# Performance work log

Hardware: AMD Instinct MI355X
Metric: run time of the kernel (lower is better)

The kernel has to match this reference:

```python
import jax, jax.numpy as jnp
import numpy as np

B, S, D = 1, 4096, 512
QK_DIM, N_HEADS = 512, 8
HEAD_DIM = QK_DIM // N_HEADS


def setup_inputs() -> dict:
    key = jax.random.key(0)
    ks = jax.random.split(key, 9)
    s_in = 1.0 / np.sqrt(D)
    s_v = 1.0 / np.sqrt(QK_DIM)
    return {
        "x": jax.random.normal(ks[0], (B, S, D), dtype=jnp.float32),
        # torch nn.Linear convention: weight (out_features, in_features)
        "Wq": jax.random.uniform(ks[1], (QK_DIM, D), jnp.float32, -s_in, s_in),
        "bq": jax.random.uniform(ks[2], (QK_DIM,), jnp.float32, -s_in, s_in),
        "Wk": jax.random.uniform(ks[3], (QK_DIM, D), jnp.float32, -s_in, s_in),
        "bk": jax.random.uniform(ks[4], (QK_DIM,), jnp.float32, -s_in, s_in),
        "Wv": jax.random.uniform(ks[5], (QK_DIM, D), jnp.float32, -s_in, s_in),
        "bv": jax.random.uniform(ks[6], (QK_DIM,), jnp.float32, -s_in, s_in),
        "Wo": jax.random.uniform(ks[7], (D, QK_DIM), jnp.float32, -s_v, s_v),
        "bo": jax.random.uniform(ks[8], (D,), jnp.float32, -s_v, s_v),
    }


def reference(x, Wq, bq, Wk, bk, Wv, bv, Wo, bo):
    # Faithful to source: tokens flattened over batch*seq before head split.
    n = x.shape[0] * x.shape[1]  # B*S
    Q = (x @ Wq.T + bq).reshape(n, N_HEADS, HEAD_DIM).transpose(1, 0, 2)  # (H, N, hd)
    K = (x @ Wk.T + bk).reshape(n, N_HEADS, HEAD_DIM).transpose(1, 0, 2)
    V = (x @ Wv.T + bv).reshape(n, N_HEADS, HEAD_DIM).transpose(1, 0, 2)
    scores = jnp.einsum("hnd,hmd->hnm", Q, K) / np.sqrt(HEAD_DIM).astype(np.float32)
    attn = jax.nn.softmax(scores, axis=-1)                # (H, N, N) materialized
    ctx = jnp.einsum("hnm,hmd->hnd", attn, V)             # (H, N, hd)
    ctx = ctx.transpose(1, 0, 2).reshape(n, QK_DIM)       # (N, qk_dim)
    return ctx @ Wo.T + bo                                # (N, input_dim)
```

## Files before the change

### kernel.cpp

```cpp
#include <hip/hip_runtime.h>
#include <math.h>

#define N_TOK 4096
#define DMODEL 512
#define NH 8
#define HD 64

typedef __attribute__((ext_vector_type(4))) float f32x4;
typedef __attribute__((ext_vector_type(8))) _Float16 f16x8;
typedef __attribute__((ext_vector_type(4))) _Float16 f16x4;

#define MFMA16(A, B, C) __builtin_amdgcn_mfma_f32_16x16x32_f16(A, B, C, 0, 0, 0)

__global__ __launch_bounds__(256) void cast_x(const float* __restrict__ x,
                                              _Float16* __restrict__ X16) {
    int i = (blockIdx.x * 256 + threadIdx.x) * 8;
    f32x4 a = *(const f32x4*)&x[i];
    f32x4 b = *(const f32x4*)&x[i + 4];
    f16x8 o = {(_Float16)a[0], (_Float16)a[1], (_Float16)a[2], (_Float16)a[3],
               (_Float16)b[0], (_Float16)b[1], (_Float16)b[2], (_Float16)b[3]};
    *(f16x8*)&X16[i] = o;
}

__global__ __launch_bounds__(256) void qkv_gemm(const _Float16* __restrict__ X16,
                                                const float* __restrict__ Wq,
                                                const float* __restrict__ bq,
                                                const float* __restrict__ Wk,
                                                const float* __restrict__ bk,
                                                const float* __restrict__ Wv,
                                                const float* __restrict__ bv,
                                                _Float16* __restrict__ Q16,
                                                _Float16* __restrict__ K16,
                                                _Float16* __restrict__ VT16) {
    __shared__ __align__(16) _Float16 As[128][72];
    __shared__ __align__(16) _Float16 Ws[64][72];
    int z = blockIdx.z;
    const float* W = (z == 0) ? Wq : (z == 1) ? Wk : Wv;
    const float* bias = (z == 0) ? bq : (z == 1) ? bk : bv;

    int n0 = blockIdx.x * 128, o0 = blockIdx.y * 64;
    int t = threadIdx.x;
    int w = t >> 6, l = t & 63, quad = l >> 4, ln = l & 15;
    int sr = t >> 3, sc = (t & 7) * 8;
    int wr = t >> 2, wc = (t & 3) * 16;

    const _Float16* Abase = X16 + (size_t)n0 * DMODEL;
    const float* Wbase = W + (size_t)o0 * DMODEL;

    f32x4 acc[2][4] = {};

    f16x8 pa[4];
    f32x4 pw[4];
#pragma unroll
    for (int r = 0; r < 4; r++) pa[r] = *(const f16x8*)&Abase[(size_t)(sr + r * 32) * DMODEL + sc];
#pragma unroll
    for (int r = 0; r < 4; r++) pw[r] = *(const f32x4*)&Wbase[(size_t)wr * DMODEL + wc + r * 4];

    for (int k0 = 0; k0 < DMODEL; k0 += 64) {
        __syncthreads();
#pragma unroll
        for (int r = 0; r < 4; r++) *(f16x8*)&As[sr + r * 32][sc] = pa[r];
        {
            f16x8 w0 = {(_Float16)pw[0][0], (_Float16)pw[0][1], (_Float16)pw[0][2],
                        (_Float16)pw[0][3], (_Float16)pw[1][0], (_Float16)pw[1][1],
                        (_Float16)pw[1][2], (_Float16)pw[1][3]};
            f16x8 w1 = {(_Float16)pw[2][0], (_Float16)pw[2][1], (_Float16)pw[2][2],
                        (_Float16)pw[2][3], (_Float16)pw[3][0], (_Float16)pw[3][1],
                        (_Float16)pw[3][2], (_Float16)pw[3][3]};
            *(f16x8*)&Ws[wr][wc] = w0;
            *(f16x8*)&Ws[wr][wc + 8] = w1;
        }
        __syncthreads();

        int k1 = k0 + 64;
        if (k1 < DMODEL) {
#pragma unroll
            for (int r = 0; r < 4; r++)
                pa[r] = *(const f16x8*)&Abase[(size_t)(sr + r * 32) * DMODEL + k1 + sc];
#pragma unroll
            for (int r = 0; r < 4; r++)
                pw[r] = *(const f32x4*)&Wbase[(size_t)wr * DMODEL + k1 + wc + r * 4];
        }

#pragma unroll
        for (int ks = 0; ks < 2; ks++) {
            f16x8 af0 = *(const f16x8*)&As[w * 32 + ln][ks * 32 + quad * 8];
            f16x8 af1 = *(const f16x8*)&As[w * 32 + 16 + ln][ks * 32 + quad * 8];
#pragma unroll
            for (int c = 0; c < 4; c++) {
                f16x8 bf = *(const f16x8*)&Ws[c * 16 + ln][ks * 32 + quad * 8];
                acc[0][c] = MFMA16(af0, bf, acc[0][c]);
                acc[1][c] = MFMA16(af1, bf, acc[1][c]);
            }
        }
    }

    int h = o0 >> 6;
    const float QS = 0.125f * 1.44269504088896340736f;

    if (z < 2) {
        float sc_ = (z == 0) ? QS : 1.0f;
#pragma unroll
        for (int c = 0; c < 4; c++) {
            float bv_ = bias[o0 + c * 16 + ln];
#pragma unroll
            for (int rt = 0; rt < 2; rt++)
#pragma unroll
                for (int i = 0; i < 4; i++) {
                    int lr = w * 32 + rt * 16 + quad * 4 + i;
                    As[lr][c * 16 + ln] = (_Float16)((acc[rt][c][i] + bv_) * sc_);
                }
        }
        __syncthreads();
        _Float16* dst = (z == 0) ? Q16 : K16;
#pragma unroll
        for (int k = 0; k < 4; k++) {
            int row = k * 32 + (t >> 3), col = (t & 7) * 8;
            *(f16x8*)&dst[((size_t)h * N_TOK + n0 + row) * HD + col] =
                *(const f16x8*)&As[row][col];
        }
    } else {
        __syncthreads();
        _Float16(*Et)[136] = (_Float16(*)[136]) & As[0][0];
#pragma unroll
        for (int c = 0; c < 4; c++) {
            float bv_ = bias[o0 + c * 16 + ln];
#pragma unroll
            for (int rt = 0; rt < 2; rt++)
#pragma unroll
                for (int i = 0; i < 4; i++) {
                    int np = (w >> 1) * 64 + (quad * 4 + i) * 4 + (w & 1) * 2 + rt;
                    Et[c * 16 + ln][np] = (_Float16)(acc[rt][c][i] + bv_);
                }
        }
        __syncthreads();
#pragma unroll
        for (int k = 0; k < 4; k++) {
            int d = k * 16 + (t >> 4), col = (t & 15) * 8;
            *(f16x8*)&VT16[((size_t)h * HD + d) * N_TOK + n0 + col] =
                *(const f16x8*)&Et[d][col];
        }
    }
}

__global__ __launch_bounds__(1024) void flash_mfma(const _Float16* __restrict__ Q16,
                                                   const _Float16* __restrict__ K16,
                                                   const _Float16* __restrict__ VT16,
                                                   _Float16* __restrict__ OP,
                                                   float* __restrict__ LS) {
    __shared__ __align__(16) _Float16 Ks[2][64][72];
    __shared__ __align__(16) _Float16 Vs[2][64][72];
    __shared__ __align__(16) _Float16 Ps[16][32][72];

    int t = threadIdx.x;
    int w = t >> 6, l = t & 63, quad = l >> 4, ln = l & 15;
    int bid = blockIdx.x;
    int h = bid & 7;
    int qt = (bid >> 3) & 7;
    int s = bid >> 6;
    int q0 = qt * 512 + w * 32;
    int m_start = s * 1024;

    f16x8 qf[2][2];
#pragma unroll
    for (int rt = 0; rt < 2; rt++) {
        const _Float16* qp = &Q16[((size_t)h * N_TOK + q0 + rt * 16 + ln) * HD + quad * 8];
        qf[rt][0] = *(const f16x8*)qp;
        qf[rt][1] = *(const f16x8*)(qp + 32);
    }

    f32x4 oacc[2][4] = {};
    f32x4 lsum[2] = {};

    const _Float16* kbase = K16 + (size_t)h * N_TOK * HD;
    const _Float16* vbase = VT16 + (size_t)h * HD * N_TOK;
    int g = t >> 9, tt = t & 511;
    int srow = tt >> 3, scol = (tt & 7) * 8;

    f16x8 pkv;
    if (g == 0)
        pkv = *(const f16x8*)(kbase + (size_t)(m_start + srow) * HD + scol);
    else
        pkv = *(const f16x8*)(vbase + (size_t)srow * N_TOK + m_start + scol);

    for (int it = 0; it < 16; it++) {
        int m0 = m_start + it * 64;
        int p = it & 1;
        if (g == 0)
            *(f16x8*)&Ks[p][srow][scol] = pkv;
        else
            *(f16x8*)&Vs[p][srow][scol] = pkv;
        __syncthreads();

        if (it < 15) {
            int m1 = m0 + 64;
            if (g == 0)
                pkv = *(const f16x8*)(kbase + (size_t)(m1 + srow) * HD + scol);
            else
                pkv = *(const f16x8*)(vbase + (size_t)srow * N_TOK + m1 + scol);
        }

        f16x8 kb[4][2];
#pragma unroll
        for (int c = 0; c < 4; c++) {
            kb[c][0] = *(const f16x8*)&Ks[p][c * 16 + ln][quad * 8];
            kb[c][1] = *(const f16x8*)&Ks[p][c * 16 + ln][32 + quad * 8];
        }
#pragma unroll
        for (int rt = 0; rt < 2; rt++) {
            f32x4 sacc[4] = {};
#pragma unroll
            for (int c = 0; c < 4; c++) {
                sacc[c] = MFMA16(qf[rt][0], kb[c][0], sacc[c]);
                sacc[c] = MFMA16(qf[rt][1], kb[c][1], sacc[c]);
            }
#pragma unroll
            for (int i = 0; i < 4; i++) {
                float p0 = __builtin_exp2f(sacc[0][i]);
                float p1 = __builtin_exp2f(sacc[1][i]);
                float p2 = __builtin_exp2f(sacc[2][i]);
                float p3 = __builtin_exp2f(sacc[3][i]);
                lsum[rt][i] += (p0 + p1) + (p2 + p3);
                f16x4 pvv = {(_Float16)p0, (_Float16)p1, (_Float16)p2, (_Float16)p3};
                *(f16x4*)&Ps[w][rt * 16 + quad * 4 + i][ln * 4] = pvv;
            }
        }
        f16x8 vb[4][2];
#pragma unroll
        for (int c = 0; c < 4; c++) {
            vb[c][0] = *(const f16x8*)&Vs[p][c * 16 + ln][quad * 8];
            vb[c][1] = *(const f16x8*)&Vs[p][c * 16 + ln][32 + quad * 8];
        }
#pragma unroll
        for (int rt = 0; rt < 2; rt++) {
            f16x8 a0 = *(const f16x8*)&Ps[w][rt * 16 + ln][quad * 8];
            f16x8 a1 = *(const f16x8*)&Ps[w][rt * 16 + ln][32 + quad * 8];
#pragma unroll
            for (int c = 0; c < 4; c++) {
                oacc[rt][c] = MFMA16(a0, vb[c][0], oacc[rt][c]);
                oacc[rt][c] = MFMA16(a1, vb[c][1], oacc[rt][c]);
            }
        }
    }

#pragma unroll
    for (int d = 1; d < 16; d <<= 1)
#pragma unroll
        for (int rt = 0; rt < 2; rt++)
#pragma unroll
            for (int i = 0; i < 4; i++) lsum[rt][i] += __shfl_xor(lsum[rt][i], d, 64);

    _Float16* obase = OP + (size_t)s * N_TOK * DMODEL;
#pragma unroll
    for (int rt = 0; rt < 2; rt++)
#pragma unroll
        for (int c = 0; c < 4; c++)
#pragma unroll
            for (int i = 0; i < 4; i++) {
                int r = q0 + rt * 16 + quad * 4 + i;
                obase[(size_t)r * DMODEL + h * HD + c * 16 + ln] = (_Float16)oacc[rt][c][i];
            }
    if (ln == 0) {
#pragma unroll
        for (int rt = 0; rt < 2; rt++)
#pragma unroll
            for (int i = 0; i < 4; i++) {
                int r = q0 + rt * 16 + quad * 4 + i;
                LS[((size_t)s * NH + h) * N_TOK + r] = lsum[rt][i];
            }
    }
}

__global__ __launch_bounds__(256) void combine(const _Float16* __restrict__ OP,
                                               const float* __restrict__ LS,
                                               _Float16* __restrict__ CTX16) {
    const size_t PSTR = (size_t)N_TOK * DMODEL;
    int idx = blockIdx.x * 256 + threadIdx.x;
    int col8 = idx & 63;
    int n = idx >> 6;
    int h = col8 >> 3;
    const float* ls = LS + (size_t)h * N_TOK + n;
    float lt = (ls[0] + ls[NH * N_TOK]) + (ls[2 * NH * N_TOK] + ls[3 * NH * N_TOK]);
    float inv = 1.0f / lt;
    size_t base = (size_t)n * DMODEL + col8 * 8;
    f16x8 a0 = *(const f16x8*)&OP[base];
    f16x8 a1 = *(const f16x8*)&OP[PSTR + base];
    f16x8 a2 = *(const f16x8*)&OP[2 * PSTR + base];
    f16x8 a3 = *(const f16x8*)&OP[3 * PSTR + base];
    f16x8 o;
#pragma unroll
    for (int j = 0; j < 8; j++)
        o[j] = (_Float16)((((float)a0[j] + (float)a1[j]) + ((float)a2[j] + (float)a3[j])) * inv);
    *(f16x8*)&CTX16[base] = o;
}

__global__ __launch_bounds__(256) void out_gemm(const _Float16* __restrict__ A,
                                                const float* __restrict__ Wo,
                                                const float* __restrict__ bo,
                                                float* __restrict__ out) {
    __shared__ __align__(16) _Float16 As[64][72];
    __shared__ __align__(16) _Float16 Ws[64][72];
    int n0 = blockIdx.x * 64, o0 = blockIdx.y * 64;
    int t = threadIdx.x;
    int w = t >> 6, l = t & 63, quad = l >> 4, ln = l & 15;
    int sr = t >> 2, sc = (t & 3) * 16;

    const _Float16* Abase = A + (size_t)n0 * DMODEL;
    const float* Wbase = Wo + (size_t)o0 * DMODEL;

    f32x4 acc[4] = {};

    f16x8 pa0 = *(const f16x8*)&Abase[(size_t)sr * DMODEL + sc];
    f16x8 pa1 = *(const f16x8*)&Abase[(size_t)sr * DMODEL + sc + 8];
    f32x4 pw[4];
#pragma unroll
    for (int r = 0; r < 4; r++) pw[r] = *(const f32x4*)&Wbase[(size_t)sr * DMODEL + sc + r * 4];

    for (int k0 = 0; k0 < DMODEL; k0 += 64) {
        __syncthreads();
        *(f16x8*)&As[sr][sc] = pa0;
        *(f16x8*)&As[sr][sc + 8] = pa1;
        {
            f16x8 w0 = {(_Float16)pw[0][0], (_Float16)pw[0][1], (_Float16)pw[0][2],
                        (_Float16)pw[0][3], (_Float16)pw[1][0], (_Float16)pw[1][1],
                        (_Float16)pw[1][2], (_Float16)pw[1][3]};
            f16x8 w1 = {(_Float16)pw[2][0], (_Float16)pw[2][1], (_Float16)pw[2][2],
                        (_Float16)pw[2][3], (_Float16)pw[3][0], (_Float16)pw[3][1],
                        (_Float16)pw[3][2], (_Float16)pw[3][3]};
            *(f16x8*)&Ws[sr][sc] = w0;
            *(f16x8*)&Ws[sr][sc + 8] = w1;
        }
        __syncthreads();

        int k1 = k0 + 64;
        if (k1 < DMODEL) {
            pa0 = *(const f16x8*)&Abase[(size_t)sr * DMODEL + k1 + sc];
            pa1 = *(const f16x8*)&Abase[(size_t)sr * DMODEL + k1 + sc + 8];
#pragma unroll
            for (int r = 0; r < 4; r++)
                pw[r] = *(const f32x4*)&Wbase[(size_t)sr * DMODEL + k1 + sc + r * 4];
        }

#pragma unroll
        for (int ks = 0; ks < 2; ks++) {
            f16x8 af = *(const f16x8*)&As[w * 16 + ln][ks * 32 + quad * 8];
#pragma unroll
            for (int c = 0; c < 4; c++) {
                f16x8 bf = *(const f16x8*)&Ws[c * 16 + ln][ks * 32 + quad * 8];
                acc[c] = MFMA16(af, bf, acc[c]);
            }
        }
    }

#pragma unroll
    for (int c = 0; c < 4; c++) {
        float bv_ = bo[o0 + c * 16 + ln];
#pragma unroll
        for (int i = 0; i < 4; i++) {
            int r = n0 + w * 16 + quad * 4 + i;
            out[(size_t)r * DMODEL + o0 + c * 16 + ln] = acc[c][i] + bv_;
        }
    }
}

extern "C" void kernel_launch(void* const* d_in, const int* in_sizes, int n_in,
                              void* d_out, int out_size, void* d_ws, size_t ws_size,
                              hipStream_t stream) {
    const float* x  = (const float*)d_in[0];
    const float* Wq = (const float*)d_in[1];
    const float* bq = (const float*)d_in[2];
    const float* Wk = (const float*)d_in[3];
    const float* bk = (const float*)d_in[4];
    const float* Wv = (const float*)d_in[5];
    const float* bv = (const float*)d_in[6];
    const float* Wo = (const float*)d_in[7];
    const float* bo = (const float*)d_in[8];
    float* out = (float*)d_out;

    char* ws = (char*)d_ws;
    _Float16* X16  = (_Float16*)(ws);
    _Float16* Q16  = (_Float16*)(ws + (4u << 20));
    _Float16* K16  = (_Float16*)(ws + (8u << 20));
    _Float16* VT16 = (_Float16*)(ws + (12u << 20));
    _Float16* OP   = (_Float16*)(ws + (16u << 20));
    float*    LSp  = (float*)   (ws + (32u << 20));
    _Float16* CTX  = (_Float16*)(ws + (33u << 20));

    cast_x<<<1024, 256, 0, stream>>>(x, X16);

    qkv_gemm<<<dim3(32, 8, 3), 256, 0, stream>>>(X16, Wq, bq, Wk, bk, Wv, bv,
                                                 Q16, K16, VT16);

    flash_mfma<<<dim3(256), 1024, 0, stream>>>(Q16, K16, VT16, OP, LSp);

    combine<<<1024, 256, 0, stream>>>(OP, LSp, CTX);

    out_gemm<<<dim3(64, 8), 256, 0, stream>>>(CTX, Wo, bo, out);
}
```

Measured before the change: 155.2 us.

## Fuse split-KV combine into output GEMM and merge QKV projections per block

The separate combine kernel is removed. The output GEMM now loads the four split partial outputs and their row sums, normalizes them in registers and stages the result as its A tile, so the intermediate context buffer round trip and one launch go away. The QKV GEMM now computes Q, K and V in one 768-thread block that shares a single staged X tile across the three weight matrices, and both GEMMs switch to double-buffered shared memory with one barrier per k-step. In exchange, the output GEMM reads four times as much A data per k-step and both kernels use larger blocks and more shared memory, which can lower occupancy.

```diff
diff --git a/kernel.cpp b/kernel.cpp
--- a/kernel.cpp
+++ b/kernel.cpp
@@ -22,7 +22,7 @@
     *(f16x8*)&X16[i] = o;
 }
 
-__global__ __launch_bounds__(256) void qkv_gemm(const _Float16* __restrict__ X16,
+__global__ __launch_bounds__(768) void qkv_gemm(const _Float16* __restrict__ X16,
                                                 const float* __restrict__ Wq,
                                                 const float* __restrict__ bq,
                                                 const float* __restrict__ Wk,
@@ -32,113 +32,154 @@
                                                 _Float16* __restrict__ Q16,
                                                 _Float16* __restrict__ K16,
                                                 _Float16* __restrict__ VT16) {
-    __shared__ __align__(16) _Float16 As[128][72];
-    __shared__ __align__(16) _Float16 Ws[64][72];
-    int z = blockIdx.z;
-    const float* W = (z == 0) ? Wq : (z == 1) ? Wk : Wv;
-    const float* bias = (z == 0) ? bq : (z == 1) ? bk : bv;
-
-    int n0 = blockIdx.x * 128, o0 = blockIdx.y * 64;
+    __shared__ __align__(16) _Float16 smem[46080];
+    _Float16* AsB = smem;
+    _Float16* WsB = smem + 18432;
+
     int t = threadIdx.x;
     int w = t >> 6, l = t & 63, quad = l >> 4, ln = l & 15;
-    int sr = t >> 3, sc = (t & 7) * 8;
-    int wr = t >> 2, wc = (t & 3) * 16;
+    int z = w >> 2, ww = w & 3;
+    int n0 = blockIdx.x * 128, o0 = blockIdx.y * 64;
+    int h = o0 >> 6;
+
+    const float* biasz = (z == 0) ? bq : (z == 1) ? bk : bv;
+
+    f32x4 acc[2][4] = {};
+
+    bool isA = (t < 256);
+    int asr = t >> 3, asc = (t & 7) * 8;
+    int tt = t - 256;
+    int wr = tt >> 3, wc = (tt & 7) * 8;
 
     const _Float16* Abase = X16 + (size_t)n0 * DMODEL;
-    const float* Wbase = W + (size_t)o0 * DMODEL;
-
-    f32x4 acc[2][4] = {};
+    const float* W0 = Wq + (size_t)o0 * DMODEL;
+    const float* W1 = Wk + (size_t)o0 * DMODEL;
+    const float* W2 = Wv + (size_t)o0 * DMODEL;
 
     f16x8 pa[4];
-    f32x4 pw[4];
-#pragma unroll
-    for (int r = 0; r < 4; r++) pa[r] = *(const f16x8*)&Abase[(size_t)(sr + r * 32) * DMODEL + sc];
-#pragma unroll
-    for (int r = 0; r < 4; r++) pw[r] = *(const f32x4*)&Wbase[(size_t)wr * DMODEL + wc + r * 4];
-
-    for (int k0 = 0; k0 < DMODEL; k0 += 64) {
+    f32x4 pw[3][2];
+    if (isA) {
+#pragma unroll
+        for (int r = 0; r < 4; r++)
+            pa[r] = *(const f16x8*)&Abase[(size_t)(asr + r * 32) * DMODEL + asc];
+    } else {
+        pw[0][0] = *(const f32x4*)&W0[(size_t)wr * DMODEL + wc];
+        pw[0][1] = *(const f32x4*)&W0[(size_t)wr * DMODEL + wc + 4];
+        pw[1][0] = *(const f32x4*)&W1[(size_t)wr * DMODEL + wc];
+        pw[1][1] = *(const f32x4*)&W1[(size_t)wr * DMODEL + wc + 4];
+        pw[2][0] = *(const f32x4*)&W2[(size_t)wr * DMODEL + wc];
+        pw[2][1] = *(const f32x4*)&W2[(size_t)wr * DMODEL + wc + 4];
+    }
+
+    for (int it = 0; it < 8; it++) {
+        int p = it & 1;
+        if (isA) {
+#pragma unroll
+            for (int r = 0; r < 4; r++)
+                *(f16x8*)&AsB[(size_t)(p * 128 + asr + r * 32) * 72 + asc] = pa[r];
+        } else {
+#pragma unroll
+            for (int zt = 0; zt < 3; zt++) {
+                f16x8 wv_ = {(_Float16)pw[zt][0][0], (_Float16)pw[zt][0][1],
+                             (_Float16)pw[zt][0][2], (_Float16)pw[zt][0][3],
+                             (_Float16)pw[zt][1][0], (_Float16)pw[zt][1][1],
+                             (_Float16)pw[zt][1][2], (_Float16)pw[zt][1][3]};
+                *(f16x8*)&WsB[(size_t)((p * 3 + zt) * 64 + wr) * 72 + wc] = wv_;
+            }
+        }
         __syncthreads();
-#pragma unroll
-        for (int r = 0; r < 4; r++) *(f16x8*)&As[sr + r * 32][sc] = pa[r];
-        {
-            f16x8 w0 = {(_Float16)pw[0][0], (_Float16)pw[0][1], (_Float16)pw[0][2],
-                        (_Float16)pw[0][3], (_Float16)pw[1][0], (_Float16)pw[1][1],
-                        (_Float16)pw[1][2], (_Float16)pw[1][3]};
-            f16x8 w1 = {(_Float16)pw[2][0], (_Float16)pw[2][1], (_Float16)pw[2][2],
-                        (_Float16)pw[2][3], (_Float16)pw[3][0], (_Float16)pw[3][1],
-                        (_Float16)pw[3][2], (_Float16)pw[3][3]};
-            *(f16x8*)&Ws[wr][wc] = w0;
-            *(f16x8*)&Ws[wr][wc + 8] = w1;
-        }
-        __syncthreads();
-
-        int k1 = k0 + 64;
+
+        int k1 = (it + 1) * 64;
         if (k1 < DMODEL) {
-#pragma unroll
-            for (int r = 0; r < 4; r++)
-                pa[r] = *(const f16x8*)&Abase[(size_t)(sr + r * 32) * DMODEL + k1 + sc];
-#pragma unroll
-            for (int r = 0; r < 4; r++)
-                pw[r] = *(const f32x4*)&Wbase[(size_t)wr * DMODEL + k1 + wc + r * 4];
+            if (isA) {
+#pragma unroll
+                for (int r = 0; r < 4; r++)
+                    pa[r] = *(const f16x8*)&Abase[(size_t)(asr + r * 32) * DMODEL + k1 + asc];
+            } else {
+                pw[0][0] = *(const f32x4*)&W0[(size_t)wr * DMODEL + k1 + wc];
+                pw[0][1] = *(const f32x4*)&W0[(size_t)wr * DMODEL + k1 + wc + 4];
+                pw[1][0] = *(const f32x4*)&W1[(size_t)wr * DMODEL + k1 + wc];
+                pw[1][1] = *(const f32x4*)&W1[(size_t)wr * DMODEL + k1 + wc + 4];
+                pw[2][0] = *(const f32x4*)&W2[(size_t)wr * DMODEL + k1 + wc];
+                pw[2][1] = *(const f32x4*)&W2[(size_t)wr * DMODEL + k1 + wc + 4];
+            }
         }
 
 #pragma unroll
         for (int ks = 0; ks < 2; ks++) {
-            f16x8 af0 = *(const f16x8*)&As[w * 32 + ln][ks * 32 + quad * 8];
-            f16x8 af1 = *(const f16x8*)&As[w * 32 + 16 + ln][ks * 32 + quad * 8];
+            f16x8 af0 = *(const f16x8*)&AsB[(size_t)(p * 128 + ww * 32 + ln) * 72 +
+                                            ks * 32 + quad * 8];
+            f16x8 af1 = *(const f16x8*)&AsB[(size_t)(p * 128 + ww * 32 + 16 + ln) * 72 +
+                                            ks * 32 + quad * 8];
 #pragma unroll
             for (int c = 0; c < 4; c++) {
-                f16x8 bf = *(const f16x8*)&Ws[c * 16 + ln][ks * 32 + quad * 8];
+                f16x8 bf = *(const f16x8*)&WsB[(size_t)((p * 3 + z) * 64 + c * 16 + ln) * 72 +
+                                               ks * 32 + quad * 8];
                 acc[0][c] = MFMA16(af0, bf, acc[0][c]);
                 acc[1][c] = MFMA16(af1, bf, acc[1][c]);
             }
         }
     }
 
-    int h = o0 >> 6;
+    __syncthreads();
+
     const float QS = 0.125f * 1.44269504088896340736f;
+    _Float16* Qs = smem;
+    _Float16* Ksep = smem + 9216;
+    _Float16* Vt = smem + 18432;
 
     if (z < 2) {
+        _Float16* st = (z == 0) ? Qs : Ksep;
         float sc_ = (z == 0) ? QS : 1.0f;
 #pragma unroll
         for (int c = 0; c < 4; c++) {
-            float bv_ = bias[o0 + c * 16 + ln];
+            float bv_ = biasz[o0 + c * 16 + ln];
 #pragma unroll
             for (int rt = 0; rt < 2; rt++)
 #pragma unroll
                 for (int i = 0; i < 4; i++) {
-                    int lr = w * 32 + rt * 16 + quad * 4 + i;
-                    As[lr][c * 16 + ln] = (_Float16)((acc[rt][c][i] + bv_) * sc_);
+                    int lr = ww * 32 + rt * 16 + quad * 4 + i;
+                    st[(size_t)lr * 72 + c * 16 + ln] =
+                        (_Float16)((acc[rt][c][i] + bv_) * sc_);
                 }
         }
-        __syncthreads();
-        _Float16* dst = (z == 0) ? Q16 : K16;
+    } else {
+#pragma unroll
+        for (int c = 0; c < 4; c++) {
+            float bv_ = biasz[o0 + c * 16 + ln];
+#pragma unroll
+            for (int rt = 0; rt < 2; rt++)
+#pragma unroll
+                for (int i = 0; i < 4; i++) {
+                    int np = (ww >> 1) * 64 + (quad * 4 + i) * 4 + (ww & 1) * 2 + rt;
+                    Vt[(size_t)(c * 16 + ln) * 136 + np] = (_Float16)(acc[rt][c][i] + bv_);
+                }
+        }
+    }
+    __syncthreads();
+
+    if (t < 256) {
 #pragma unroll
         for (int k = 0; k < 4; k++) {
             int row = k * 32 + (t >> 3), col = (t & 7) * 8;
-            *(f16x8*)&dst[((size_t)h * N_TOK + n0 + row) * HD + col] =
-                *(const f16x8*)&As[row][col];
+            *(f16x8*)&Q16[((size_t)h * N_TOK + n0 + row) * HD + col] =
+                *(const f16x8*)&Qs[(size_t)row * 72 + col];
+        }
+    } else if (t < 512) {
+        int u = t - 256;
+#pragma unroll
+        for (int k = 0; k < 4; k++) {
+            int row = k * 32 + (u >> 3), col = (u & 7) * 8;
+            *(f16x8*)&K16[((size_t)h * N_TOK + n0 + row) * HD + col] =
+                *(const f16x8*)&Ksep[(size_t)row * 72 + col];
         }
     } else {
-        __syncthreads();
-        _Float16(*Et)[136] = (_Float16(*)[136]) & As[0][0];
-#pragma unroll
-        for (int c = 0; c < 4; c++) {
-            float bv_ = bias[o0 + c * 16 + ln];
-#pragma unroll
-            for (int rt = 0; rt < 2; rt++)
-#pragma unroll
-                for (int i = 0; i < 4; i++) {
-                    int np = (w >> 1) * 64 + (quad * 4 + i) * 4 + (w & 1) * 2 + rt;
-                    Et[c * 16 + ln][np] = (_Float16)(acc[rt][c][i] + bv_);
-                }
-        }
-        __syncthreads();
+        int u = t - 512;
 #pragma unroll
         for (int k = 0; k < 4; k++) {
-            int d = k * 16 + (t >> 4), col = (t & 15) * 8;
+            int d = k * 16 + (u >> 4), col = (u & 15) * 8;
             *(f16x8*)&VT16[((size_t)h * HD + d) * N_TOK + n0 + col] =
-                *(const f16x8*)&Et[d][col];
+                *(const f16x8*)&Vt[(size_t)d * 136 + col];
         }
     }
 }
@@ -271,82 +312,88 @@
     }
 }
 
-__global__ __launch_bounds__(256) void combine(const _Float16* __restrict__ OP,
-                                               const float* __restrict__ LS,
-                                               _Float16* __restrict__ CTX16) {
-    const size_t PSTR = (size_t)N_TOK * DMODEL;
-    int idx = blockIdx.x * 256 + threadIdx.x;
-    int col8 = idx & 63;
-    int n = idx >> 6;
-    int h = col8 >> 3;
-    const float* ls = LS + (size_t)h * N_TOK + n;
-    float lt = (ls[0] + ls[NH * N_TOK]) + (ls[2 * NH * N_TOK] + ls[3 * NH * N_TOK]);
-    float inv = 1.0f / lt;
-    size_t base = (size_t)n * DMODEL + col8 * 8;
-    f16x8 a0 = *(const f16x8*)&OP[base];
-    f16x8 a1 = *(const f16x8*)&OP[PSTR + base];
-    f16x8 a2 = *(const f16x8*)&OP[2 * PSTR + base];
-    f16x8 a3 = *(const f16x8*)&OP[3 * PSTR + base];
-    f16x8 o;
-#pragma unroll
-    for (int j = 0; j < 8; j++)
-        o[j] = (_Float16)((((float)a0[j] + (float)a1[j]) + ((float)a2[j] + (float)a3[j])) * inv);
-    *(f16x8*)&CTX16[base] = o;
-}
-
-__global__ __launch_bounds__(256) void out_gemm(const _Float16* __restrict__ A,
+__global__ __launch_bounds__(512) void out_gemm(const _Float16* __restrict__ OP,
+                                                const float* __restrict__ LS,
                                                 const float* __restrict__ Wo,
                                                 const float* __restrict__ bo,
                                                 float* __restrict__ out) {
-    __shared__ __align__(16) _Float16 As[64][72];
-    __shared__ __align__(16) _Float16 Ws[64][72];
-    int n0 = blockIdx.x * 64, o0 = blockIdx.y * 64;
+    __shared__ __align__(16) _Float16 smem[27648];
+    _Float16* AsB = smem;
+    _Float16* WsB = smem + 18432;
+
     int t = threadIdx.x;
     int w = t >> 6, l = t & 63, quad = l >> 4, ln = l & 15;
+    int n0 = blockIdx.x * 128, o0 = blockIdx.y * 64;
     int sr = t >> 2, sc = (t & 3) * 16;
-
-    const _Float16* Abase = A + (size_t)n0 * DMODEL;
+    int wr = t >> 3, wc = (t & 7) * 8;
+    const size_t PSTR = (size_t)N_TOK * DMODEL;
+
+    f32x4 acc[4] = {};
+
     const float* Wbase = Wo + (size_t)o0 * DMODEL;
 
-    f32x4 acc[4] = {};
-
-    f16x8 pa0 = *(const f16x8*)&Abase[(size_t)sr * DMODEL + sc];
-    f16x8 pa1 = *(const f16x8*)&Abase[(size_t)sr * DMODEL + sc + 8];
-    f32x4 pw[4];
-#pragma unroll
-    for (int r = 0; r < 4; r++) pw[r] = *(const f32x4*)&Wbase[(size_t)sr * DMODEL + sc + r * 4];
-
-    for (int k0 = 0; k0 < DMODEL; k0 += 64) {
+    f16x8 pa[4][2];
+    float lt;
+    f32x4 pw0, pw1;
+    {
+        size_t base = (size_t)(n0 + sr) * DMODEL + sc;
+#pragma unroll
+        for (int s_ = 0; s_ < 4; s_++) {
+            pa[s_][0] = *(const f16x8*)&OP[s_ * PSTR + base];
+            pa[s_][1] = *(const f16x8*)&OP[s_ * PSTR + base + 8];
+        }
+        const float* ls = LS + n0 + sr;
+        lt = (ls[0] + ls[NH * N_TOK]) + (ls[2 * NH * N_TOK] + ls[3 * NH * N_TOK]);
+        pw0 = *(const f32x4*)&Wbase[(size_t)wr * DMODEL + wc];
+        pw1 = *(const f32x4*)&Wbase[(size_t)wr * DMODEL + wc + 4];
+    }
+
+    for (int it = 0; it < 8; it++) {
+        int p = it & 1;
+        {
+            float inv = 1.0f / lt;
+            f16x8 s0, s1;
+#pragma unroll
+            for (int j = 0; j < 8; j++) {
+                s0[j] = (_Float16)(
+                    ((((float)pa[0][0][j] + (float)pa[1][0][j]) +
+                      ((float)pa[2][0][j] + (float)pa[3][0][j]))) * inv);
+                s1[j] = (_Float16)(
+                    ((((float)pa[0][1][j] + (float)pa[1][1][j]) +
+                      ((float)pa[2][1][j] + (float)pa[3][1][j]))) * inv);
+            }
+            *(f16x8*)&AsB[(size_t)(p * 128 + sr) * 72 + sc] = s0;
+            *(f16x8*)&AsB[(size_t)(p * 128 + sr) * 72 + sc + 8] = s1;
+            f16x8 wv_ = {(_Float16)pw0[0], (_Float16)pw0[1], (_Float16)pw0[2],
+                         (_Float16)pw0[3], (_Float16)pw1[0], (_Float16)pw1[1],
+                         (_Float16)pw1[2], (_Float16)pw1[3]};
+            *(f16x8*)&WsB[(size_t)(p * 64 + wr) * 72 + wc] = wv_;
+        }
         __syncthreads();
-        *(f16x8*)&As[sr][sc] = pa0;
-        *(f16x8*)&As[sr][sc + 8] = pa1;
-        {
-            f16x8 w0 = {(_Float16)pw[0][0], (_Float16)pw[0][1], (_Float16)pw[0][2],
-                        (_Float16)pw[0][3], (_Float16)pw[1][0], (_Float16)pw[1][1],
-                        (_Float16)pw[1][2], (_Float16)pw[1][3]};
-            f16x8 w1 = {(_Float16)pw[2][0], (_Float16)pw[2][1], (_Float16)pw[2][2],
-                        (_Float16)pw[2][3], (_Float16)pw[3][0], (_Float16)pw[3][1],
-                        (_Float16)pw[3][2], (_Float16)pw[3][3]};
-            *(f16x8*)&Ws[sr][sc] = w0;
-            *(f16x8*)&Ws[sr][sc + 8] = w1;
-        }
-        __syncthreads();
-
-        int k1 = k0 + 64;
+
+        int k1 = (it + 1) * 64;
         if (k1 < DMODEL) {
-            pa0 = *(const f16x8*)&Abase[(size_t)sr * DMODEL + k1 + sc];
-            pa1 = *(const f16x8*)&Abase[(size_t)sr * DMODEL + k1 + sc + 8];
-#pragma unroll
-            for (int r = 0; r < 4; r++)
-                pw[r] = *(const f32x4*)&Wbase[(size_t)sr * DMODEL + k1 + sc + r * 4];
+            int h1 = k1 >> 6;
+            size_t base = (size_t)(n0 + sr) * DMODEL + k1 + sc;
+#pragma unroll
+            for (int s_ = 0; s_ < 4; s_++) {
+                pa[s_][0] = *(const f16x8*)&OP[s_ * PSTR + base];
+                pa[s_][1] = *(const f16x8*)&OP[s_ * PSTR + base + 8];
+            }
+            const float* ls = LS + (size_t)h1 * N_TOK + n0 + sr;
+            lt = (ls[0] + ls[NH * N_TOK]) + (ls[2 * NH * N_TOK] + ls[3 * NH * N_TOK]);
+            pw0 = *(const f32x4*)&Wbase[(size_t)wr * DMODEL + k1 + wc];
+            pw1 = *(const f32x4*)&Wbase[(size_t)wr * DMODEL + k1 + wc + 4];
         }
 
 #pragma unroll
         for (int ks = 0; ks < 2; ks++) {
-            f16x8 af = *(const f16x8*)&As[w * 16 + ln][ks * 32 + quad * 8];
+            f16x8 af = *(const f16x8*)&AsB[(size_t)(p * 128 + w * 16 + ln) * 72 +
+                                           ks * 32 + quad * 8];
 #pragma unroll
             for (int c = 0; c < 4; c++) {
-                f16x8 bf = *(const f16x8*)&Ws[c * 16 + ln][ks * 32 + quad * 8];
+                f16x8 bf = *(const f16x8*)&WsB[(size_t)(p * 64 + c * 16 + ln) * 72 +
+                                               ks * 32 + quad * 8];
                 acc[c] = MFMA16(af, bf, acc[c]);
             }
         }
@@ -384,16 +431,13 @@
     _Float16* VT16 = (_Float16*)(ws + (12u << 20));
     _Float16* OP   = (_Float16*)(ws + (16u << 20));
     float*    LSp  = (float*)   (ws + (32u << 20));
-    _Float16* CTX  = (_Float16*)(ws + (33u << 20));
 
     cast_x<<<1024, 256, 0, stream>>>(x, X16);
 
-    qkv_gemm<<<dim3(32, 8, 3), 256, 0, stream>>>(X16, Wq, bq, Wk, bk, Wv, bv,
-                                                 Q16, K16, VT16);
+    qkv_gemm<<<dim3(32, 8), 768, 0, stream>>>(X16, Wq, bq, Wk, bk, Wv, bv,
+                                              Q16, K16, VT16);
 
     flash_mfma<<<dim3(256), 1024, 0, stream>>>(Q16, K16, VT16, OP, LSp);
 
-    combine<<<1024, 256, 0, stream>>>(OP, LSp, CTX);
-
-    out_gemm<<<dim3(64, 8), 256, 0, stream>>>(CTX, Wo, bo, out);
+    out_gemm<<<dim3(32, 8), 512, 0, stream>>>(OP, LSp, Wo, bo, out);
 }
```

Measured after the change: 154.9 us. About the same (-0.2%).
